# Kernel optimization log

Measured on AMD Instinct MI355X. Metric: run time of the kernel, lower is better.

## Reference

```python
import jax, jax.numpy as jnp
import numpy as np

N_USER = 100000
N_ITEM = 100000
SUPP = 10000
B = 1024
L = 50
S = 256
H = 4
E = 64
HID = 64


def setup_inputs() -> dict:
    key = jax.random.key(0)
    ks = jax.random.split(key, 32)
    f32 = jnp.float32
    inp = {}
    # forward int args
    inp["x"] = jax.random.randint(ks[0], (B, 2), 0, N_USER)
    inp["src_his"] = jax.random.randint(ks[1], (B, L), 0, N_ITEM)
    inp["src_hl"] = jax.random.randint(ks[2], (B,), 0, L)
    inp["tgt_his"] = jax.random.randint(ks[3], (B, L), 0, N_ITEM)
    inp["tgt_hl"] = jax.random.randint(ks[4], (B,), 0, L)
    # precomputed neighbor sampling: [2 get_user_emb calls, H heads, B, S]
    inp["sample_idx"] = jax.random.randint(ks[5], (2, H, B, S), 0, SUPP)
    inp["supp_users"] = jax.random.randint(ks[6], (SUPP,), 0, N_USER)
    # embedding tables (xavier-ish small scale)
    inp["src_user_emb"] = jax.random.normal(ks[7], (N_USER, E), f32) * 0.1
    inp["src_item_emb"] = jax.random.normal(ks[8], (N_ITEM, E), f32) * 0.1
    inp["tgt_user_emb"] = jax.random.normal(ks[9], (N_USER, E), f32) * 0.1
    inp["tgt_item_emb"] = jax.random.normal(ks[10], (N_ITEM, E), f32) * 0.1
    # attention / aggregation weights, stored [in, out]
    s = 1.0 / np.sqrt(E)
    inp["W_att_w"] = jax.random.normal(ks[11], (E, E), f32) * s
    inp["W_att_b"] = jnp.full((E,), 0.1, f32)
    inp["W_agg_w"] = jax.random.normal(ks[12], (E, E), f32) * s
    # per-head GAT projections, batched over heads
    inp["Wq"] = jax.random.normal(ks[13], (H, E, E), f32) * s
    inp["Wk"] = jax.random.normal(ks[14], (H, E, E), f32) * s
    inp["Wv"] = jax.random.normal(ks[15], (H, E, E), f32) * s
    inp["W_out"] = jax.random.normal(ks[16], (H * E, E), f32) * (1.0 / np.sqrt(H * E))
    # scoring MLP
    inp["l1_w"] = jax.random.normal(ks[17], (2 * E, HID), f32) * (1.0 / np.sqrt(2 * E))
    inp["l1_b"] = jnp.full((HID,), 0.1, f32)
    inp["l2_w"] = jax.random.normal(ks[18], (HID, E), f32) * (1.0 / np.sqrt(HID))
    inp["l2_b"] = jnp.full((E,), 0.1, f32)
    inp["l3_w"] = jax.random.normal(ks[19], (E, 1), f32) * s
    inp["l3_b"] = jnp.full((1,), 0.1, f32)
    return inp


def reference(x, src_his, src_hl, tgt_his, tgt_hl, sample_idx, supp_users,
              src_user_emb, src_item_emb, tgt_user_emb, tgt_item_emb,
              W_att_w, W_att_b, W_agg_w, Wq, Wk, Wv, W_out,
              l1_w, l1_b, l2_w, l2_b, l3_w, l3_b):
    user_id = x[:, 0]
    item_id = x[:, 1]

    def user_fea_encode(his, hl, user_table):
        # NOTE: original always gathers from src_model.item_embedding (even for tgt)
        Lh = his.shape[1]
        valid = jnp.arange(Lh)[None, :] < hl[:, None]          # [B,L]
        hist = src_item_emb[his] * valid[..., None]             # [B,L,E], padded rows zeroed
        u = user_table[user_id]                                 # [B,E]
        keyt = jnp.tanh(hist @ W_att_w + W_att_b)               # [B,L,E]
        pad = hist.sum(-1) == 0                                 # [B,L]
        att = jnp.einsum('ble,be->bl', keyt, u)
        # faithful masked_softmax: masked scores set to 0 BEFORE exp (exp(0)=1 still contributes)
        att = jnp.where(pad, 0.0, att)
        e = jnp.exp(att)
        att = e / (jnp.sum(e, axis=1, keepdims=True) + 1e-12)
        out = jnp.einsum('bl,ble->be', att, hist)
        return out @ W_agg_w                                    # W_agg has no bias

    def get_user_emb(fea, idx):
        # idx: [H,B,S] indices into supp_users; all heads batched in one einsum chain
        neigh = tgt_user_emb[supp_users[idx]]                   # [H,B,S,E]
        q = jnp.einsum('be,heo->hbo', fea, Wq)                  # [H,B,O]
        k = jnp.einsum('hbse,heo->hbso', neigh, Wk)             # [H,B,S,O]
        attn = jax.nn.softmax(jnp.einsum('hbo,hbso->hbs', q, k), axis=-1)
        ctx = jnp.einsum('hbs,hbso->hbo', attn, k)              # weighted sum over neighbors
        g = jnp.einsum('hbo,hop->hbp', ctx, Wv)                 # [H,B,O]
        g = jnp.transpose(g, (1, 0, 2)).reshape(fea.shape[0], -1)  # concat heads -> [B,H*O]
        return g @ W_out

    user_src_fea = user_fea_encode(src_his, src_hl, src_user_emb)
    user_emb = get_user_emb(user_src_fea, sample_idx[0])
    item_emb = tgt_item_emb[item_id]
    user_tgt_fea = user_fea_encode(tgt_his, tgt_hl, tgt_user_emb)
    hybrid_tgt_emb = get_user_emb(user_tgt_fea, sample_idx[1])

    x_t = jnp.concatenate([hybrid_tgt_emb, item_emb], axis=1)
    x1_t = jnp.tanh(x_t @ l1_w + l1_b)
    x2_t = jnp.tanh(x1_t @ l2_w + l2_b)
    x3_t = (x2_t @ l3_w + l3_b).reshape(-1)

    output = jnp.sum(user_emb * item_emb, axis=1)
    out_emb_s = user_emb * item_emb
    # (output, output_t, out_emb_s, out_emb_t); train=False branch (sim/domain heads are None)
    return (output, x3_t, out_emb_s, x2_t)
```

## Files before the change

kernel.cpp:

```cpp
#include <hip/hip_runtime.h>

constexpr int B    = 1024;
constexpr int L    = 50;
constexpr int S    = 256;
constexpr int H    = 4;
constexpr int E    = 64;
constexpr int HID  = 64;
constexpr int SUPP = 10000;

__device__ __forceinline__ float lanebc(float v, int l) {
    return __int_as_float(__builtin_amdgcn_readlane(__float_as_int(v), l));
}

__global__ __launch_bounds__(256) void pre_kernel(
    const int* __restrict__ x,
    const int* __restrict__ src_his,
    const int* __restrict__ src_hl,
    const int* __restrict__ tgt_his,
    const int* __restrict__ tgt_hl,
    const float* __restrict__ item_emb,
    const float* __restrict__ src_user_emb,
    const float* __restrict__ tgt_user_emb,
    const int* __restrict__ supp_users,
    const float* __restrict__ W_att_w,
    const float* __restrict__ W_att_b,
    const float* __restrict__ W_agg_w,
    const float* __restrict__ Wq,
    const float* __restrict__ Wk,
    float* __restrict__ qout,
    float* __restrict__ K_supp)
{
    const int tid  = threadIdx.x;
    const int lane = tid & 63;
    const int wave = tid >> 6;

    if (blockIdx.y == 2) {
        const int h = wave;
        float wcol[E];
#pragma unroll
        for (int i = 0; i < E; i++) wcol[i] = Wk[h * E * E + i * E + lane];

#pragma unroll 2
        for (int j = blockIdx.x; j < SUPP; j += gridDim.x) {
            const int u = supp_users[j];
            const float ev = tgt_user_emb[(size_t)u * E + lane];
            float acc = 0.0f;
#pragma unroll
            for (int i = 0; i < E; i++) acc += lanebc(ev, i) * wcol[i];
            K_supp[((size_t)h * SUPP + j) * E + lane] = acc;
        }
        return;
    }

    __shared__ float sHist[L * E];
    __shared__ float sAtt[L];
    __shared__ float sPart[4][E];
    __shared__ float sOut[E];

    const int b    = blockIdx.x;
    const int call = blockIdx.y;

    const int* his = call ? tgt_his : src_his;
    const int* hl  = call ? tgt_hl  : src_hl;
    const float* user_table = call ? tgt_user_emb : src_user_emb;

    float wcol[E];
#pragma unroll
    for (int i = 0; i < E; i++) wcol[i] = W_att_w[i * E + lane];

    const int uid    = x[2 * b];
    const float uv   = user_table[(size_t)uid * E + lane];
    const float bias = W_att_b[lane];
    const int hlen   = hl[b];

    for (int l = wave; l < L; l += 4) {
        const int it = his[b * L + l];
        const float hv = (l < hlen) ? item_emb[(size_t)it * E + lane] : 0.0f;
        sHist[l * E + lane] = hv;
        float a = bias;
#pragma unroll
        for (int i = 0; i < E; i++) a += lanebc(hv, i) * wcol[i];
        float part = tanhf(a) * uv;
        float hsum = hv;
#pragma unroll
        for (int off = 32; off; off >>= 1) {
            part += __shfl_xor(part, off);
            hsum += __shfl_xor(hsum, off);
        }
        if (lane == 0) sAtt[l] = (hsum == 0.0f) ? 0.0f : part;
    }
    __syncthreads();

    if (wave == 0) {
        float v = (lane < L) ? expf(sAtt[lane]) : 0.0f;
        float s = v;
#pragma unroll
        for (int off = 32; off; off >>= 1) s += __shfl_xor(s, off);
        const float denom = s + 1e-12f;
        if (lane < L) sAtt[lane] = v / denom;
    }
    __syncthreads();

    float c = 0.0f;
    for (int l = wave; l < L; l += 4) c += sAtt[l] * sHist[l * E + lane];
    sPart[wave][lane] = c;
    __syncthreads();
    if (tid < E) sOut[tid] = sPart[0][tid] + sPart[1][tid] + sPart[2][tid] + sPart[3][tid];
    __syncthreads();

    float g = 0.0f;
#pragma unroll
    for (int k = 0; k < 16; k++) {
        const int i = wave * 16 + k;
        g += sOut[i] * W_agg_w[i * E + lane];
    }
    sPart[wave][lane] = g;
    __syncthreads();

    const float fval = sPart[0][lane] + sPart[1][lane] + sPart[2][lane] + sPart[3][lane];
    const float* Wqh = Wq + wave * E * E;
    float qacc = 0.0f;
#pragma unroll
    for (int i = 0; i < E; i++) qacc += lanebc(fval, i) * Wqh[i * E + lane];
    qout[(((call * H) + wave) * B + b) * E + lane] = qacc;
}

__global__ __launch_bounds__(256) void attn_kernel(
    const int* __restrict__ sample_idx,
    const float* __restrict__ K_supp,
    const float* __restrict__ qarr,
    const float* __restrict__ Wv,
    float* __restrict__ gout)
{
    __shared__ float sRed[8];
    __shared__ float sCtx[4][E];
    __shared__ float sC[E];
    __shared__ float sG[4][E];

    const int b    = blockIdx.x;
    const int h    = blockIdx.y;
    const int call = blockIdx.z;
    const int tid  = threadIdx.x;
    const int lane = tid & 63;
    const int wave = tid >> 6;
    const int u    = lane & 15;
    const int rsub = lane >> 4;
    const int s0   = wave * 64;

    const int* idx = sample_idx + (((call * H) + h) * B + b) * S;
    const float* Kh = K_supp + (size_t)h * SUPP * E;
    const float4 qu = *(const float4*)(qarr + ((size_t)(((call * H) + h) * B + b)) * E + 4 * u);

    float4 kreg[16];
    float mylogit = 0.0f;
#pragma unroll
    for (int i = 0; i < 16; i++) {
        const int j = idx[s0 + 4 * i + rsub];
        kreg[i] = *(const float4*)(Kh + (size_t)j * E + 4 * u);
        float part = kreg[i].x * qu.x + kreg[i].y * qu.y
                   + kreg[i].z * qu.z + kreg[i].w * qu.w;
#pragma unroll
        for (int off = 1; off < 16; off <<= 1) part += __shfl_xor(part, off);
        mylogit = (u == i) ? part : mylogit;
    }

    float m = mylogit;
#pragma unroll
    for (int off = 32; off; off >>= 1) m = fmaxf(m, __shfl_xor(m, off));
    if (lane == 0) sRed[wave] = m;
    __syncthreads();
    const float mx = fmaxf(fmaxf(sRed[0], sRed[1]), fmaxf(sRed[2], sRed[3]));
    const float ex = expf(mylogit - mx);
    float sm = ex;
#pragma unroll
    for (int off = 32; off; off >>= 1) sm += __shfl_xor(sm, off);
    if (lane == 0) sRed[4 + wave] = sm;
    __syncthreads();
    const float denom = sRed[4] + sRed[5] + sRed[6] + sRed[7];
    const float pval = ex / denom;

    float4 cacc = make_float4(0.0f, 0.0f, 0.0f, 0.0f);
#pragma unroll
    for (int i = 0; i < 16; i++) {
        const float p = __shfl(pval, (lane & 48) + i);
        cacc.x += p * kreg[i].x;
        cacc.y += p * kreg[i].y;
        cacc.z += p * kreg[i].z;
        cacc.w += p * kreg[i].w;
    }
#pragma unroll
    for (int off = 16; off <= 32; off <<= 1) {
        cacc.x += __shfl_xor(cacc.x, off);
        cacc.y += __shfl_xor(cacc.y, off);
        cacc.z += __shfl_xor(cacc.z, off);
        cacc.w += __shfl_xor(cacc.w, off);
    }
    if (lane < 16) *(float4*)(&sCtx[wave][u * 4]) = cacc;
    __syncthreads();
    if (wave == 0) {
        sC[lane] = sCtx[0][lane] + sCtx[1][lane] + sCtx[2][lane] + sCtx[3][lane];
    }
    __syncthreads();

    const float* Wvh = Wv + h * E * E;
    float g = 0.0f;
#pragma unroll
    for (int k = 0; k < 16; k++) {
        const int c = wave * 16 + k;
        g += sC[c] * Wvh[c * E + lane];
    }
    sG[wave][lane] = g;
    __syncthreads();
    if (wave == 0) {
        gout[((size_t)(call * B) + b) * (H * E) + h * E + lane] =
            sG[0][lane] + sG[1][lane] + sG[2][lane] + sG[3][lane];
    }
}

__global__ __launch_bounds__(256) void final_kernel(
    const int* __restrict__ x,
    const float* __restrict__ tgt_item_emb,
    const float* __restrict__ gsrc,
    const float* __restrict__ gtgt,
    const float* __restrict__ W_out,
    const float* __restrict__ l1_w,
    const float* __restrict__ l1_b,
    const float* __restrict__ l2_w,
    const float* __restrict__ l2_b,
    const float* __restrict__ l3_w,
    const float* __restrict__ l3_b,
    float* __restrict__ out)
{
    __shared__ float sPart[4][E];
    __shared__ float sHyb[E];
    __shared__ float sItem[E];
    __shared__ float sX1[HID];

    const int b    = blockIdx.x;
    const int tid  = threadIdx.x;
    const int lane = tid & 63;
    const int wave = tid >> 6;

    if (tid < E) {
        const int item = x[2 * b + 1];
        sItem[tid] = tgt_item_emb[(size_t)item * E + tid];
    }

    const float* grow = (wave < 2) ? (gsrc + (size_t)b * (H * E))
                                   : (gtgt + (size_t)b * (H * E));
    const int i0 = (wave & 1) * 128;
    float acc = 0.0f;
    for (int i = i0; i < i0 + 128; i++) {
        acc += grow[i] * W_out[i * E + lane];
    }
    sPart[wave][lane] = acc;
    __syncthreads();

    if (wave == 0) {
        const float ue = sPart[0][lane] + sPart[1][lane];
        const float prod = ue * sItem[lane];
        out[2 * B + b * E + lane] = prod;
        float s = prod;
#pragma unroll
        for (int off = 32; off; off >>= 1) s += __shfl_xor(s, off);
        if (lane == 0) out[b] = s;
    }
    if (wave == 1) {
        sHyb[lane] = sPart[2][lane] + sPart[3][lane];
    }
    __syncthreads();

    float a1 = 0.0f;
#pragma unroll
    for (int k = 0; k < 32; k++) {
        const int i = wave * 32 + k;
        const float v = (i < 64) ? sHyb[i] : sItem[i - 64];
        a1 += v * l1_w[i * HID + lane];
    }
    sPart[wave][lane] = a1;
    __syncthreads();

    if (wave == 0) {
        const float a = l1_b[lane] + sPart[0][lane] + sPart[1][lane]
                      + sPart[2][lane] + sPart[3][lane];
        sX1[lane] = tanhf(a);
    }
    __syncthreads();

    if (wave == 0) {
        float a = l2_b[lane];
#pragma unroll
        for (int i = 0; i < HID; i++) a += sX1[i] * l2_w[i * E + lane];
        const float x2 = tanhf(a);
        out[2 * B + B * E + b * E + lane] = x2;
        float p = x2 * l3_w[lane];
#pragma unroll
        for (int off = 32; off; off >>= 1) p += __shfl_xor(p, off);
        if (lane == 0) out[B + b] = p + l3_b[0];
    }
}

extern "C" void kernel_launch(void* const* d_in, const int* in_sizes, int n_in,
                              void* d_out, int out_size, void* d_ws, size_t ws_size,
                              hipStream_t stream) {
    const int*   x            = (const int*)d_in[0];
    const int*   src_his      = (const int*)d_in[1];
    const int*   src_hl       = (const int*)d_in[2];
    const int*   tgt_his      = (const int*)d_in[3];
    const int*   tgt_hl       = (const int*)d_in[4];
    const int*   sample_idx   = (const int*)d_in[5];
    const int*   supp_users   = (const int*)d_in[6];
    const float* src_user_emb = (const float*)d_in[7];
    const float* src_item_emb = (const float*)d_in[8];
    const float* tgt_user_emb = (const float*)d_in[9];
    const float* tgt_item_emb = (const float*)d_in[10];
    const float* W_att_w      = (const float*)d_in[11];
    const float* W_att_b      = (const float*)d_in[12];
    const float* W_agg_w      = (const float*)d_in[13];
    const float* Wq           = (const float*)d_in[14];
    const float* Wk           = (const float*)d_in[15];
    const float* Wv           = (const float*)d_in[16];
    const float* W_out        = (const float*)d_in[17];
    const float* l1_w         = (const float*)d_in[18];
    const float* l1_b         = (const float*)d_in[19];
    const float* l2_w         = (const float*)d_in[20];
    const float* l2_b         = (const float*)d_in[21];
    const float* l3_w         = (const float*)d_in[22];
    const float* l3_b         = (const float*)d_in[23];

    float* ws      = (float*)d_ws;
    float* qarr    = ws;
    float* K_supp  = qarr + 2 * H * B * E;
    float* garr    = K_supp + H * SUPP * E;
    float* out     = (float*)d_out;

    pre_kernel<<<dim3(B, 3), 256, 0, stream>>>(
        x, src_his, src_hl, tgt_his, tgt_hl, src_item_emb,
        src_user_emb, tgt_user_emb, supp_users,
        W_att_w, W_att_b, W_agg_w, Wq, Wk, qarr, K_supp);
    attn_kernel<<<dim3(B, H, 2), 256, 0, stream>>>(
        sample_idx, K_supp, qarr, Wv, garr);
    final_kernel<<<dim3(B), 256, 0, stream>>>(
        x, tgt_item_emb, garr, garr + B * H * E, W_out,
        l1_w, l1_b, l2_w, l2_b, l3_w, l3_b, out);
}
```

Baseline: 276.8 us.

## Replace readlane matvecs with LDS float4 broadcasts, fast tanh/exp, XCD-aware attn grid

Matrix-vector products that used readlane broadcasts now stage vectors in shared memory and read them as float4 with four independent accumulators, in the Wk precompute, attention scoring, W_agg, Wq and W_out paths. tanhf and expf are swapped for exp/rcp-based fast versions. The attention grid is flattened so the low three bits of the block index select head and call, aiming at L2 locality per XCD for the K_supp slice. The aim is to cut the scalar-broadcast and transcendental cost, at the price of extra syncthreads and a small loss of precision.

New measurement: 259.4 us. 1.07x faster.

```diff
diff --git a/kernel.cpp b/kernel.cpp
--- a/kernel.cpp
+++ b/kernel.cpp
@@ -8,8 +8,10 @@
 constexpr int HID  = 64;
 constexpr int SUPP = 10000;
 
-__device__ __forceinline__ float lanebc(float v, int l) {
-    return __int_as_float(__builtin_amdgcn_readlane(__float_as_int(v), l));
+__device__ __forceinline__ float tanh_fast(float x) {
+    const float xc = fminf(fmaxf(x, -15.0f), 15.0f);
+    const float e  = __expf(2.0f * xc);
+    return (e - 1.0f) * __builtin_amdgcn_rcpf(e + 1.0f);
 }
 
 __global__ __launch_bounds__(256) void pre_kernel(
@@ -35,27 +37,44 @@
     const int wave = tid >> 6;
 
     if (blockIdx.y == 2) {
+        __shared__ __align__(16) float sEv[4][E];
         const int h = wave;
-        float wcol[E];
-#pragma unroll
-        for (int i = 0; i < E; i++) wcol[i] = Wk[h * E * E + i * E + lane];
-
-#pragma unroll 2
-        for (int j = blockIdx.x; j < SUPP; j += gridDim.x) {
-            const int u = supp_users[j];
-            const float ev = tgt_user_emb[(size_t)u * E + lane];
-            float acc = 0.0f;
-#pragma unroll
-            for (int i = 0; i < E; i++) acc += lanebc(ev, i) * wcol[i];
-            K_supp[((size_t)h * SUPP + j) * E + lane] = acc;
+        float wkc[E];
+#pragma unroll
+        for (int i = 0; i < E; i++) wkc[i] = Wk[h * E * E + i * E + lane];
+
+        for (int j0 = blockIdx.x * 4; j0 < SUPP; j0 += gridDim.x * 4) {
+            const int jm = j0 + wave;
+            if (jm < SUPP) {
+                const int u = supp_users[jm];
+                sEv[wave][lane] = tgt_user_emb[(size_t)u * E + lane];
+            }
+            __syncthreads();
+            const int mmax = min(4, SUPP - j0);
+            for (int m = 0; m < mmax; m++) {
+                const float4* e4 = (const float4*)&sEv[m][0];
+                float a0 = 0.0f, a1 = 0.0f, a2 = 0.0f, a3 = 0.0f;
+#pragma unroll
+                for (int k = 0; k < 16; k++) {
+                    const float4 v = e4[k];
+                    a0 += v.x * wkc[4 * k + 0];
+                    a1 += v.y * wkc[4 * k + 1];
+                    a2 += v.z * wkc[4 * k + 2];
+                    a3 += v.w * wkc[4 * k + 3];
+                }
+                K_supp[((size_t)h * SUPP + j0 + m) * E + lane] = (a0 + a1) + (a2 + a3);
+            }
+            __syncthreads();
         }
         return;
     }
 
-    __shared__ float sHist[L * E];
+    __shared__ __align__(16) float sHist[L * E];
+    __shared__ float sHs[L];
     __shared__ float sAtt[L];
     __shared__ float sPart[4][E];
-    __shared__ float sOut[E];
+    __shared__ __align__(16) float sOut[E];
+    __shared__ __align__(16) float sFea[E];
 
     const int b    = blockIdx.x;
     const int call = blockIdx.y;
@@ -77,22 +96,34 @@
         const int it = his[b * L + l];
         const float hv = (l < hlen) ? item_emb[(size_t)it * E + lane] : 0.0f;
         sHist[l * E + lane] = hv;
-        float a = bias;
-#pragma unroll
-        for (int i = 0; i < E; i++) a += lanebc(hv, i) * wcol[i];
-        float part = tanhf(a) * uv;
-        float hsum = hv;
-#pragma unroll
-        for (int off = 32; off; off >>= 1) {
-            part += __shfl_xor(part, off);
-            hsum += __shfl_xor(hsum, off);
+        float hs = hv;
+#pragma unroll
+        for (int off = 32; off; off >>= 1) hs += __shfl_xor(hs, off);
+        if (lane == 0) sHs[l] = hs;
+    }
+    __syncthreads();
+
+    for (int l = wave; l < L; l += 4) {
+        const float4* hrow = (const float4*)&sHist[l * E];
+        float a0 = 0.0f, a1 = 0.0f, a2 = 0.0f, a3 = 0.0f;
+#pragma unroll
+        for (int k = 0; k < 16; k++) {
+            const float4 h4 = hrow[k];
+            a0 += h4.x * wcol[4 * k + 0];
+            a1 += h4.y * wcol[4 * k + 1];
+            a2 += h4.z * wcol[4 * k + 2];
+            a3 += h4.w * wcol[4 * k + 3];
         }
-        if (lane == 0) sAtt[l] = (hsum == 0.0f) ? 0.0f : part;
-    }
-    __syncthreads();
-
-    if (wave == 0) {
-        float v = (lane < L) ? expf(sAtt[lane]) : 0.0f;
+        float part = tanh_fast((a0 + a1) + (a2 + a3) + bias) * uv;
+#pragma unroll
+        for (int off = 32; off; off >>= 1) part += __shfl_xor(part, off);
+        const float hs = sHs[l];
+        if (lane == 0) sAtt[l] = (hs == 0.0f) ? 0.0f : part;
+    }
+    __syncthreads();
+
+    if (wave == 0) {
+        float v = (lane < L) ? __expf(sAtt[lane]) : 0.0f;
         float s = v;
 #pragma unroll
         for (int off = 32; off; off >>= 1) s += __shfl_xor(s, off);
@@ -108,21 +139,38 @@
     if (tid < E) sOut[tid] = sPart[0][tid] + sPart[1][tid] + sPart[2][tid] + sPart[3][tid];
     __syncthreads();
 
-    float g = 0.0f;
-#pragma unroll
-    for (int k = 0; k < 16; k++) {
-        const int i = wave * 16 + k;
-        g += sOut[i] * W_agg_w[i * E + lane];
-    }
-    sPart[wave][lane] = g;
-    __syncthreads();
-
-    const float fval = sPart[0][lane] + sPart[1][lane] + sPart[2][lane] + sPart[3][lane];
-    const float* Wqh = Wq + wave * E * E;
-    float qacc = 0.0f;
-#pragma unroll
-    for (int i = 0; i < E; i++) qacc += lanebc(fval, i) * Wqh[i * E + lane];
-    qout[(((call * H) + wave) * B + b) * E + lane] = qacc;
+    {
+        const float4* o4 = (const float4*)&sOut[wave * 16];
+        float g0 = 0.0f, g1 = 0.0f, g2 = 0.0f, g3 = 0.0f;
+#pragma unroll
+        for (int k = 0; k < 4; k++) {
+            const float4 v = o4[k];
+            const int i = wave * 16 + 4 * k;
+            g0 += v.x * W_agg_w[(i + 0) * E + lane];
+            g1 += v.y * W_agg_w[(i + 1) * E + lane];
+            g2 += v.z * W_agg_w[(i + 2) * E + lane];
+            g3 += v.w * W_agg_w[(i + 3) * E + lane];
+        }
+        sPart[wave][lane] = (g0 + g1) + (g2 + g3);
+    }
+    __syncthreads();
+    if (tid < E) sFea[tid] = sPart[0][tid] + sPart[1][tid] + sPart[2][tid] + sPart[3][tid];
+    __syncthreads();
+
+    {
+        const float* Wqh = Wq + wave * E * E;
+        const float4* f4p = (const float4*)sFea;
+        float q0 = 0.0f, q1 = 0.0f, q2 = 0.0f, q3 = 0.0f;
+#pragma unroll
+        for (int k = 0; k < 16; k++) {
+            const float4 f4 = f4p[k];
+            q0 += f4.x * Wqh[(4 * k + 0) * E + lane];
+            q1 += f4.y * Wqh[(4 * k + 1) * E + lane];
+            q2 += f4.z * Wqh[(4 * k + 2) * E + lane];
+            q3 += f4.w * Wqh[(4 * k + 3) * E + lane];
+        }
+        qout[(((call * H) + wave) * B + b) * E + lane] = (q0 + q1) + (q2 + q3);
+    }
 }
 
 __global__ __launch_bounds__(256) void attn_kernel(
@@ -137,9 +185,11 @@
     __shared__ float sC[E];
     __shared__ float sG[4][E];
 
-    const int b    = blockIdx.x;
-    const int h    = blockIdx.y;
-    const int call = blockIdx.z;
+    const int n    = blockIdx.x;
+    const int xcd  = n & 7;
+    const int h    = xcd >> 1;
+    const int call = xcd & 1;
+    const int b    = n >> 3;
     const int tid  = threadIdx.x;
     const int lane = tid & 63;
     const int wave = tid >> 6;
@@ -170,7 +220,7 @@
     if (lane == 0) sRed[wave] = m;
     __syncthreads();
     const float mx = fmaxf(fmaxf(sRed[0], sRed[1]), fmaxf(sRed[2], sRed[3]));
-    const float ex = expf(mylogit - mx);
+    const float ex = __expf(mylogit - mx);
     float sm = ex;
 #pragma unroll
     for (int off = 32; off; off >>= 1) sm += __shfl_xor(sm, off);
@@ -249,11 +299,20 @@
     const float* grow = (wave < 2) ? (gsrc + (size_t)b * (H * E))
                                    : (gtgt + (size_t)b * (H * E));
     const int i0 = (wave & 1) * 128;
-    float acc = 0.0f;
-    for (int i = i0; i < i0 + 128; i++) {
-        acc += grow[i] * W_out[i * E + lane];
-    }
-    sPart[wave][lane] = acc;
+    {
+        const float4* g4 = (const float4*)(grow + i0);
+        float a0 = 0.0f, a1 = 0.0f, a2 = 0.0f, a3 = 0.0f;
+#pragma unroll
+        for (int k = 0; k < 32; k++) {
+            const float4 v = g4[k];
+            const float* wr = W_out + (i0 + 4 * k) * E + lane;
+            a0 += v.x * wr[0];
+            a1 += v.y * wr[E];
+            a2 += v.z * wr[2 * E];
+            a3 += v.w * wr[3 * E];
+        }
+        sPart[wave][lane] = (a0 + a1) + (a2 + a3);
+    }
     __syncthreads();
 
     if (wave == 0) {
@@ -283,7 +342,7 @@
     if (wave == 0) {
         const float a = l1_b[lane] + sPart[0][lane] + sPart[1][lane]
                       + sPart[2][lane] + sPart[3][lane];
-        sX1[lane] = tanhf(a);
+        sX1[lane] = tanh_fast(a);
     }
     __syncthreads();
 
@@ -291,7 +350,7 @@
         float a = l2_b[lane];
 #pragma unroll
         for (int i = 0; i < HID; i++) a += sX1[i] * l2_w[i * E + lane];
-        const float x2 = tanhf(a);
+        const float x2 = tanh_fast(a);
         out[2 * B + B * E + b * E + lane] = x2;
         float p = x2 * l3_w[lane];
 #pragma unroll
@@ -338,7 +397,7 @@
         x, src_his, src_hl, tgt_his, tgt_hl, src_item_emb,
         src_user_emb, tgt_user_emb, supp_users,
         W_att_w, W_att_b, W_agg_w, Wq, Wk, qarr, K_supp);
-    attn_kernel<<<dim3(B, H, 2), 256, 0, stream>>>(
+    attn_kernel<<<dim3(B * H * 2), 256, 0, stream>>>(
         sample_idx, K_supp, qarr, Wv, garr);
     final_kernel<<<dim3(B), 256, 0, stream>>>(
         x, tgt_item_emb, garr, garr + B * H * E, W_out,
```

## Skip masked history rows, remap attention grid per XCD, batch gather loads, fast math

Applied to the files above, without the earlier changes.

The pre kernel now skips the gather and projection for history positions past the sequence length. It also folds the softmax normalisation into the weighted sum using lane broadcasts, which removes one barrier. The attention kernel flattens its grid so that the low three block bits choose head and call, intended to keep each K_supp head slice on one MI355X XCD's L2, and it issues all 16 gathers before computing. Fast exp/rcp and tanh approximations and a float4-vectorised W_out dot product are added. The accuracy risk is small, but masked rows whose embedding sums to zero are no longer treated specially.

Measured after the change: 261.4 us. 5.6% less time.

```diff
diff --git a/kernel.cpp b/kernel.cpp
--- a/kernel.cpp
+++ b/kernel.cpp
@@ -7,6 +7,12 @@
 constexpr int E    = 64;
 constexpr int HID  = 64;
 constexpr int SUPP = 10000;
+
+__device__ __forceinline__ float tanh_fast(float x) {
+    const float xc = fminf(fmaxf(x, -15.0f), 15.0f);
+    const float e  = __expf(2.0f * xc);
+    return (e - 1.0f) * __builtin_amdgcn_rcpf(e + 1.0f);
+}
 
 __device__ __forceinline__ float lanebc(float v, int l) {
     return __int_as_float(__builtin_amdgcn_readlane(__float_as_int(v), l));
@@ -53,7 +59,7 @@
     }
 
     __shared__ float sHist[L * E];
-    __shared__ float sAtt[L];
+    __shared__ float sAtt[64];
     __shared__ float sPart[4][E];
     __shared__ float sOut[E];
 
@@ -74,35 +80,32 @@
     const int hlen   = hl[b];
 
     for (int l = wave; l < L; l += 4) {
-        const int it = his[b * L + l];
-        const float hv = (l < hlen) ? item_emb[(size_t)it * E + lane] : 0.0f;
-        sHist[l * E + lane] = hv;
-        float a = bias;
-#pragma unroll
-        for (int i = 0; i < E; i++) a += lanebc(hv, i) * wcol[i];
-        float part = tanhf(a) * uv;
-        float hsum = hv;
-#pragma unroll
-        for (int off = 32; off; off >>= 1) {
-            part += __shfl_xor(part, off);
-            hsum += __shfl_xor(hsum, off);
+        if (l < hlen) {
+            const int it = his[b * L + l];
+            const float hv = item_emb[(size_t)it * E + lane];
+            sHist[l * E + lane] = hv;
+            float a = bias;
+#pragma unroll
+            for (int i = 0; i < E; i++) a += lanebc(hv, i) * wcol[i];
+            float part = tanh_fast(a) * uv;
+#pragma unroll
+            for (int off = 32; off; off >>= 1) part += __shfl_xor(part, off);
+            if (lane == 0) sAtt[l] = part;
+        } else {
+            if (lane == 0) sAtt[l] = 0.0f;
         }
-        if (lane == 0) sAtt[l] = (hsum == 0.0f) ? 0.0f : part;
-    }
-    __syncthreads();
-
-    if (wave == 0) {
-        float v = (lane < L) ? expf(sAtt[lane]) : 0.0f;
-        float s = v;
-#pragma unroll
-        for (int off = 32; off; off >>= 1) s += __shfl_xor(s, off);
-        const float denom = s + 1e-12f;
-        if (lane < L) sAtt[lane] = v / denom;
-    }
-    __syncthreads();
+    }
+    __syncthreads();
+
+    const float vex = (lane < L) ? __expf(sAtt[lane]) : 0.0f;
+    float sden = vex;
+#pragma unroll
+    for (int off = 32; off; off >>= 1) sden += __shfl_xor(sden, off);
+    const float rden = __builtin_amdgcn_rcpf(sden + 1e-12f);
 
     float c = 0.0f;
-    for (int l = wave; l < L; l += 4) c += sAtt[l] * sHist[l * E + lane];
+    for (int l = wave; l < hlen; l += 4)
+        c = fmaf(lanebc(vex, l) * rden, sHist[l * E + lane], c);
     sPart[wave][lane] = c;
     __syncthreads();
     if (tid < E) sOut[tid] = sPart[0][tid] + sPart[1][tid] + sPart[2][tid] + sPart[3][tid];
@@ -137,9 +140,11 @@
     __shared__ float sC[E];
     __shared__ float sG[4][E];
 
-    const int b    = blockIdx.x;
-    const int h    = blockIdx.y;
-    const int call = blockIdx.z;
+    const int n    = blockIdx.x;
+    const int xcd  = n & 7;
+    const int h    = xcd >> 1;
+    const int call = xcd & 1;
+    const int b    = n >> 3;
     const int tid  = threadIdx.x;
     const int lane = tid & 63;
     const int wave = tid >> 6;
@@ -151,12 +156,17 @@
     const float* Kh = K_supp + (size_t)h * SUPP * E;
     const float4 qu = *(const float4*)(qarr + ((size_t)(((call * H) + h) * B + b)) * E + 4 * u);
 
+    int jr[16];
+#pragma unroll
+    for (int i = 0; i < 16; i++) jr[i] = idx[s0 + 4 * i + rsub];
     float4 kreg[16];
+#pragma unroll
+    for (int i = 0; i < 16; i++)
+        kreg[i] = *(const float4*)(Kh + (size_t)jr[i] * E + 4 * u);
+
     float mylogit = 0.0f;
 #pragma unroll
     for (int i = 0; i < 16; i++) {
-        const int j = idx[s0 + 4 * i + rsub];
-        kreg[i] = *(const float4*)(Kh + (size_t)j * E + 4 * u);
         float part = kreg[i].x * qu.x + kreg[i].y * qu.y
                    + kreg[i].z * qu.z + kreg[i].w * qu.w;
 #pragma unroll
@@ -170,7 +180,7 @@
     if (lane == 0) sRed[wave] = m;
     __syncthreads();
     const float mx = fmaxf(fmaxf(sRed[0], sRed[1]), fmaxf(sRed[2], sRed[3]));
-    const float ex = expf(mylogit - mx);
+    const float ex = __expf(mylogit - mx);
     float sm = ex;
 #pragma unroll
     for (int off = 32; off; off >>= 1) sm += __shfl_xor(sm, off);
@@ -249,11 +259,20 @@
     const float* grow = (wave < 2) ? (gsrc + (size_t)b * (H * E))
                                    : (gtgt + (size_t)b * (H * E));
     const int i0 = (wave & 1) * 128;
-    float acc = 0.0f;
-    for (int i = i0; i < i0 + 128; i++) {
-        acc += grow[i] * W_out[i * E + lane];
-    }
-    sPart[wave][lane] = acc;
+    {
+        const float4* g4 = (const float4*)(grow + i0);
+        float a0 = 0.0f, a1 = 0.0f, a2 = 0.0f, a3 = 0.0f;
+#pragma unroll
+        for (int k = 0; k < 32; k++) {
+            const float4 v = g4[k];
+            const float* wr = W_out + (i0 + 4 * k) * E + lane;
+            a0 += v.x * wr[0];
+            a1 += v.y * wr[E];
+            a2 += v.z * wr[2 * E];
+            a3 += v.w * wr[3 * E];
+        }
+        sPart[wave][lane] = (a0 + a1) + (a2 + a3);
+    }
     __syncthreads();
 
     if (wave == 0) {
@@ -283,7 +302,7 @@
     if (wave == 0) {
         const float a = l1_b[lane] + sPart[0][lane] + sPart[1][lane]
                       + sPart[2][lane] + sPart[3][lane];
-        sX1[lane] = tanhf(a);
+        sX1[lane] = tanh_fast(a);
     }
     __syncthreads();
 
@@ -291,7 +310,7 @@
         float a = l2_b[lane];
 #pragma unroll
         for (int i = 0; i < HID; i++) a += sX1[i] * l2_w[i * E + lane];
-        const float x2 = tanhf(a);
+        const float x2 = tanh_fast(a);
         out[2 * B + B * E + b * E + lane] = x2;
         float p = x2 * l3_w[lane];
 #pragma unroll
@@ -338,7 +357,7 @@
         x, src_his, src_hl, tgt_his, tgt_hl, src_item_emb,
         src_user_emb, tgt_user_emb, supp_users,
         W_att_w, W_att_b, W_agg_w, Wq, Wk, qarr, K_supp);
-    attn_kernel<<<dim3(B, H, 2), 256, 0, stream>>>(
+    attn_kernel<<<dim3(B * H * 2), 256, 0, stream>>>(
         sample_idx, K_supp, qarr, Wv, garr);
     final_kernel<<<dim3(B), 256, 0, stream>>>(
         x, tgt_item_emb, garr, garr + B * H * E, W_out,
```
